# Kernel tuning notes

Measured on AMD Instinct MI355X. Metric: run time of the kernel, lower is better.

The kernel has to match this reference:

```python
import jax, jax.numpy as jnp
import numpy as np

NUM_CLASS = 3
LIMIT = 576.0 * 576.0   # from __init__ default limit=576*576
EPS = 1e-5              # normalize_with_limit eps
COS_EPS = 1e-8          # cosine_similarity eps
BIG = 1e9               # 'infinity' for EDT init (>> max possible squared dist)


def _edt(mask):
    """Exact Euclidean distance transform of a binary [H,W] mask.
    For nonzero pixels: distance to nearest zero pixel (scipy semantics).
    Separable squared EDT via brute-force min-plus 1D transforms."""
    H, W = mask.shape
    f = jnp.where(mask > 0, jnp.float32(BIG), jnp.float32(0.0))  # [H,W] sq dists
    jw = jnp.arange(W, dtype=jnp.float32)
    r2w = (jw[:, None] - jw[None, :]) ** 2  # [W,W] (j-k)^2
    jh = jnp.arange(H, dtype=jnp.float32)
    r2h = (jh[:, None] - jh[None, :]) ** 2  # [H,H]
    # pass along width: d[i,j] = min_k f[i,k] + (j-k)^2
    d = jnp.min(f[:, None, :] + r2w[None, :, :], axis=-1)        # [H,W]
    # pass along height: d[i,j] = min_k d[k,j] + (i-k)^2
    d = jnp.min(d.T[:, None, :] + r2h[None, :, :], axis=-1).T    # [H,W]
    return jnp.sqrt(d)


def _norm_limit(x):
    m = jnp.minimum(jnp.max(x), jnp.float32(LIMIT))
    return x / (m + jnp.float32(EPS))


def _dw(mask):
    return _norm_limit(_edt(mask))


def setup_inputs() -> dict:
    key = jax.random.key(0)
    k1, k2 = jax.random.split(key)
    B, C, H, W = 4, NUM_CLASS, 256, 256
    pred = jax.random.normal(k1, (B, C, H, W), dtype=jnp.float32)
    lab = jax.random.randint(k2, (B, H, W), 0, C, dtype=jnp.int32)
    return {"pred": pred, "lab": lab}


def reference(pred, lab):
    B, C, H, W = pred.shape
    pred_lbl = jnp.argmax(pred, axis=1)              # [B,H,W]
    lab = lab.reshape(pred_lbl.shape)

    lab_oh = jax.nn.one_hot(lab, C, dtype=jnp.float32)        # [B,H,W,C]
    pred_oh = jax.nn.one_hot(pred_lbl, C, dtype=jnp.float32)  # [B,H,W,C]
    lab_oh_c = jnp.moveaxis(lab_oh, -1, 1)           # [B,C,H,W] == getBAV masks
    pred_oh_c = jnp.moveaxis(pred_oh, -1, 1)

    # per-class distance weights (normalized EDT) -- sequential map keeps memory low
    lab_dw = jax.lax.map(_dw, lab_oh_c.reshape(B * C, H, W)).reshape(B, C, H, W)
    pred_dw = jax.lax.map(_dw, pred_oh_c.reshape(B * C, H, W)).reshape(B, C, H, W)

    # feat = [sum_c dw ; one_hot] -> [B, 1+C, H, W]
    lab_feat = jnp.concatenate([jnp.sum(lab_dw, axis=1, keepdims=True), lab_oh_c], axis=1)
    pred_feat = jnp.concatenate([jnp.sum(pred_dw, axis=1, keepdims=True), pred_oh_c], axis=1)

    # cosine similarity per pixel over the (1+C)=4 channel dim
    dot = jnp.sum(pred_feat * lab_feat, axis=1)                # [B,H,W]
    na = jnp.sqrt(jnp.sum(pred_feat * pred_feat, axis=1))
    nb = jnp.sqrt(jnp.sum(lab_feat * lab_feat, axis=1))
    sim = dot / (jnp.maximum(na, COS_EPS) * jnp.maximum(nb, COS_EPS))

    loss_b = 1.0 - jnp.mean(sim.reshape(B, -1), axis=1)        # [B]
    has_fg = jnp.sum((lab > 0).astype(jnp.int32), axis=(1, 2)) > 0
    loss = jnp.sum(jnp.where(has_fg, loss_b, 0.0)) / B
    return jnp.nan_to_num(loss, nan=0.0, posinf=1.0, neginf=0.0)
```

## Files before the change

### kernel.cpp

```cpp
#include <hip/hip_runtime.h>
#include <hip/hip_bf16.h>

#define HH 256
#define WW 256
#define BB 4
#define CC 3
#define HW 65536
#define NM 24
#define BIGF 1e9f
#define LIMITF 331776.0f
#define EPSF 1e-5f

__global__ __launch_bounds__(256) void k_rowpass(const float* __restrict__ pred,
                                                 const int* __restrict__ lab,
                                                 float* __restrict__ dbuf) {
    int blk = blockIdx.x;
    int b = blk >> 8;
    int i = blk & 255;
    int j = threadIdx.x;
    int ii = i * i;

    int lv = lab[(b << 16) + (i << 8) + j];
    const float* pb = pred + (((size_t)(b * 3)) << 16) + (i << 8) + j;
    float p0 = pb[0];
    float p1 = pb[(size_t)1 << 16];
    float p2 = pb[(size_t)2 << 16];
    int am = 0; float v = p0;
    if (p1 > v) { am = 1; v = p1; }
    if (p2 > v) { am = 2; }

    __shared__ unsigned long long zm[6][4];
    int w = threadIdx.x >> 6;
    #pragma unroll
    for (int c = 0; c < 3; ++c) {
        unsigned long long zl = __ballot(lv != c);
        unsigned long long zp = __ballot(am != c);
        if ((threadIdx.x & 63) == 0) { zm[c][w] = zl; zm[3 + c][w] = zp; }
    }
    __syncthreads();

    #pragma unroll
    for (int t = 0; t < 6; ++t) {
        int bestd = 512;
        #pragma unroll
        for (int w2 = 0; w2 < 4; ++w2) {
            unsigned long long z = zm[t][w2];
            int base = w2 << 6;
            int rel = j - base;
            unsigned long long mle;
            if (rel >= 63)      mle = ~0ULL;
            else if (rel < 0)   mle = 0ULL;
            else                mle = (2ULL << rel) - 1ULL;
            unsigned long long zl = z & mle;
            if (zl) {
                int p = base + 63 - __clzll(zl);
                int d = j - p;
                if (d < bestd) bestd = d;
            }
            unsigned long long zr = z & ~mle;
            if (zr) {
                int p = base + __ffsll(zr) - 1;
                int d = p - j;
                if (d < bestd) bestd = d;
            }
        }
        float g = (bestd >= 512) ? (BIGF + (float)ii)
                                 : (float)(bestd * bestd + ii);
        int c = (t < 3) ? t : (t - 3);
        int m = ((t < 3) ? 0 : 12) + b * 3 + c;
        dbuf[(((size_t)m) << 16) + (i << 8) + j] = g;
    }
}

__global__ __launch_bounds__(256) void k_colpass(float* __restrict__ dbuf,
                                                 float* __restrict__ blkmax) {
    int blk = blockIdx.x;
    int m = blk >> 5;
    int j0 = (blk & 31) << 3;
    __shared__ float tile[256 * 8];
    float* base = dbuf + (((size_t)m) << 16);

    #pragma unroll
    for (int it = 0; it < 8; ++it) {
        int idx = (it << 8) + threadIdx.x;
        int row = idx >> 3, jj = idx & 7;
        tile[idx] = base[(row << 8) + j0 + jj];
    }
    __syncthreads();

    int jj = threadIdx.x & 7;
    int ib = threadIdx.x >> 3;
    float acc[8], m2i[8];
    #pragma unroll
    for (int r = 0; r < 8; ++r) {
        acc[r] = 3e38f;
        m2i[r] = -2.0f * (float)(ib + (r << 5));
    }

    float kf = 0.0f;
    #pragma unroll 8
    for (int k = 0; k < 256; ++k) {
        float gk = tile[(k << 3) + jj];
        #pragma unroll
        for (int r = 0; r < 8; ++r)
            acc[r] = fminf(acc[r], fmaf(m2i[r], kf, gk));
        kf += 1.0f;
    }

    int col = j0 + jj;
    float lmax = 0.0f;
    #pragma unroll
    for (int r = 0; r < 8; ++r) {
        int i = ib + (r << 5);
        float d = acc[r] + (float)(i * i);
        base[(i << 8) + col] = d;
        lmax = fmaxf(lmax, d);
    }

    #pragma unroll
    for (int off = 32; off; off >>= 1)
        lmax = fmaxf(lmax, __shfl_down(lmax, off, 64));
    __shared__ float wmax[4];
    if ((threadIdx.x & 63) == 0) wmax[threadIdx.x >> 6] = lmax;
    __syncthreads();
    if (threadIdx.x == 0)
        blkmax[blk] = fmaxf(fmaxf(wmax[0], wmax[1]), fmaxf(wmax[2], wmax[3]));
}

__global__ __launch_bounds__(256) void k_final(const float* __restrict__ pred,
                                               const int* __restrict__ lab,
                                               const float* __restrict__ dbuf,
                                               const float* __restrict__ blkmax,
                                               float* __restrict__ psum,
                                               int* __restrict__ pfg) {
    __shared__ float inv[NM];
    if (threadIdx.x < NM) {
        const float* bm = blkmax + (threadIdx.x << 5);
        float v = 0.0f;
        #pragma unroll
        for (int s = 0; s < 32; ++s) v = fmaxf(v, bm[s]);
        inv[threadIdx.x] = 1.0f / (fminf(sqrtf(v), LIMITF) + EPSF);
    }
    __syncthreads();

    int b = blockIdx.x >> 8;
    int pix = ((blockIdx.x & 255) << 8) + threadIdx.x;

    int lv = lab[(b << 16) + pix];
    const float* pb = pred + (((size_t)(b * 3)) << 16) + pix;
    float p0 = pb[0];
    float p1 = pb[(size_t)1 << 16];
    float p2 = pb[(size_t)2 << 16];
    int am = 0; float v = p0;
    if (p1 > v) { am = 1; v = p1; }
    if (p2 > v) { am = 2; }

    float slab = 0.0f, spred = 0.0f;
    #pragma unroll
    for (int c = 0; c < 3; ++c) {
        int ml = b * 3 + c;
        float dl = dbuf[(((size_t)ml) << 16) + pix];
        slab += sqrtf(dl) * inv[ml];
        float dp = dbuf[(((size_t)(ml + 12)) << 16) + pix];
        spred += sqrtf(dp) * inv[ml + 12];
    }

    float dot = spred * slab + ((am == lv) ? 1.0f : 0.0f);
    float na = sqrtf(spred * spred + 1.0f);
    float nb = sqrtf(slab * slab + 1.0f);
    float sim = dot / (fmaxf(na, 1e-8f) * fmaxf(nb, 1e-8f));

    unsigned long long fg = __ballot(lv > 0);

    #pragma unroll
    for (int off = 32; off; off >>= 1)
        sim += __shfl_down(sim, off, 64);
    __shared__ float wsum[4];
    __shared__ int wfg[4];
    if ((threadIdx.x & 63) == 0) {
        wsum[threadIdx.x >> 6] = sim;
        wfg[threadIdx.x >> 6] = (fg != 0ULL) ? 1 : 0;
    }
    __syncthreads();
    if (threadIdx.x == 0) {
        psum[blockIdx.x] = wsum[0] + wsum[1] + wsum[2] + wsum[3];
        pfg[blockIdx.x] = wfg[0] | wfg[1] | wfg[2] | wfg[3];
    }
}

__global__ __launch_bounds__(256) void k_finalize(const float* __restrict__ psum,
                                                  const int* __restrict__ pfg,
                                                  float* __restrict__ out) {
    int t = threadIdx.x;
    int b = t >> 6, l = t & 63;
    int base = (b << 8) + l;
    float s = psum[base] + psum[base + 64] + psum[base + 128] + psum[base + 192];
    int f = pfg[base] | pfg[base + 64] | pfg[base + 128] | pfg[base + 192];
    #pragma unroll
    for (int off = 32; off; off >>= 1) {
        s += __shfl_down(s, off, 64);
        f |= __shfl_down(f, off, 64);
    }
    __shared__ float bsum[4];
    __shared__ int bfg[4];
    if (l == 0) { bsum[b] = s; bfg[b] = f; }
    __syncthreads();
    if (t == 0) {
        float loss = 0.0f;
        for (int bb = 0; bb < BB; ++bb) {
            float lb = 1.0f - bsum[bb] * (1.0f / (float)HW);
            if (bfg[bb]) loss += lb;
        }
        loss *= (1.0f / (float)BB);
        if (isnan(loss)) loss = 0.0f;
        else if (isinf(loss)) loss = (loss > 0.0f) ? 1.0f : 0.0f;
        out[0] = loss;
    }
}

extern "C" void kernel_launch(void* const* d_in, const int* in_sizes, int n_in,
                              void* d_out, int out_size, void* d_ws, size_t ws_size,
                              hipStream_t stream) {
    const float* pred = (const float*)d_in[0];
    const int*   lab  = (const int*)d_in[1];

    char* wsb = (char*)d_ws;
    float* dbuf   = (float*)wsb;
    size_t off    = (size_t)NM * HW * sizeof(float);
    float* blkmax = (float*)(wsb + off);          off += 768 * sizeof(float);
    float* psum   = (float*)(wsb + off);          off += 1024 * sizeof(float);
    int*   pfg    = (int*)  (wsb + off);

    k_rowpass <<<BB * HH,  256, 0, stream>>>(pred, lab, dbuf);
    k_colpass <<<NM * 32,  256, 0, stream>>>(dbuf, blkmax);
    k_final   <<<BB * 256, 256, 0, stream>>>(pred, lab, dbuf, blkmax, psum, pfg);
    k_finalize<<<1,        256, 0, stream>>>(psum, pfg, (float*)d_out);
}
```

Before: 89.77 us.

## Bound column-pass EDT search window by row distance and vectorize tile loads

The row pass now stores only the 1D squared distance without the i^2 offset. The column pass restricts the min-plus search for each output to a window of radius sqrt(row distance)+1 around the pixel, instead of scanning all 256 rows. The tile load uses float4 global reads into a padded shared-memory tile (stride 9). Because window sizes vary per thread, the loop can diverge. For masks with large empty regions (BIG init) the window expands back to the full range.

```diff
diff --git a/kernel.cpp b/kernel.cpp
--- a/kernel.cpp
+++ b/kernel.cpp
@@ -18,7 +18,6 @@
     int b = blk >> 8;
     int i = blk & 255;
     int j = threadIdx.x;
-    int ii = i * i;
 
     int lv = lab[(b << 16) + (i << 8) + j];
     const float* pb = pred + (((size_t)(b * 3)) << 16) + (i << 8) + j;
@@ -64,11 +63,10 @@
                 if (d < bestd) bestd = d;
             }
         }
-        float g = (bestd >= 512) ? (BIGF + (float)ii)
-                                 : (float)(bestd * bestd + ii);
+        float d1 = (bestd >= 512) ? BIGF : (float)(bestd * bestd);
         int c = (t < 3) ? t : (t - 3);
         int m = ((t < 3) ? 0 : 12) + b * 3 + c;
-        dbuf[(((size_t)m) << 16) + (i << 8) + j] = g;
+        dbuf[(((size_t)m) << 16) + (i << 8) + j] = d1;
     }
 }
 
@@ -77,44 +75,39 @@
     int blk = blockIdx.x;
     int m = blk >> 5;
     int j0 = (blk & 31) << 3;
-    __shared__ float tile[256 * 8];
+    __shared__ float tile[256 * 9];
     float* base = dbuf + (((size_t)m) << 16);
 
     #pragma unroll
-    for (int it = 0; it < 8; ++it) {
-        int idx = (it << 8) + threadIdx.x;
-        int row = idx >> 3, jj = idx & 7;
-        tile[idx] = base[(row << 8) + j0 + jj];
+    for (int it = 0; it < 2; ++it) {
+        int f = (it << 8) + threadIdx.x;
+        int row = f >> 1, half = f & 1;
+        float4 v = *(const float4*)(base + (row << 8) + j0 + (half << 2));
+        int lb = row * 9 + (half << 2);
+        tile[lb + 0] = v.x; tile[lb + 1] = v.y;
+        tile[lb + 2] = v.z; tile[lb + 3] = v.w;
     }
     __syncthreads();
 
     int jj = threadIdx.x & 7;
     int ib = threadIdx.x >> 3;
-    float acc[8], m2i[8];
-    #pragma unroll
-    for (int r = 0; r < 8; ++r) {
-        acc[r] = 3e38f;
-        m2i[r] = -2.0f * (float)(ib + (r << 5));
-    }
-
-    float kf = 0.0f;
-    #pragma unroll 8
-    for (int k = 0; k < 256; ++k) {
-        float gk = tile[(k << 3) + jj];
-        #pragma unroll
-        for (int r = 0; r < 8; ++r)
-            acc[r] = fminf(acc[r], fmaf(m2i[r], kf, gk));
-        kf += 1.0f;
-    }
-
-    int col = j0 + jj;
     float lmax = 0.0f;
+
     #pragma unroll
     for (int r = 0; r < 8; ++r) {
         int i = ib + (r << 5);
-        float d = acc[r] + (float)(i * i);
-        base[(i << 8) + col] = d;
-        lmax = fmaxf(lmax, d);
+        float di = tile[i * 9 + jj];
+        float acc = di;
+        int R = (int)sqrtf(di) + 1;
+        if (R > 255) R = 255;
+        int k0 = i - R; if (k0 < 0) k0 = 0;
+        int k1 = i + R; if (k1 > 255) k1 = 255;
+        for (int k = k0; k <= k1; ++k) {
+            float dk = (float)(k - i);
+            acc = fminf(acc, fmaf(dk, dk, tile[k * 9 + jj]));
+        }
+        base[(i << 8) + j0 + jj] = acc;
+        lmax = fmaxf(lmax, acc);
     }
 
     #pragma unroll
```

Result: faster. 84.34 us (-6.0%).
